# Performance work log

Hardware: AMD Instinct MI355X
Metric: run time of the kernel (lower is better)

Reference implementation:

```python
import jax, jax.numpy as jnp
import numpy as np

UNITS, N, S = 256, 64, 4
BATCH, T = 64, 1024


def setup_inputs() -> dict:
    key = jax.random.key(0)
    k0, k1, k2, k3 = jax.random.split(key, 4)
    return {
        "inputs": jax.random.uniform(k0, (BATCH, T, S), dtype=jnp.float32),
        "transition_kernel": jax.random.normal(k1, (UNITS, N, N), dtype=jnp.float32),
        "emission_kernel": jax.random.normal(k2, (UNITS, N, S), dtype=jnp.float32),
        "init_kernel": jax.random.normal(k3, (UNITS, N), dtype=jnp.float32),
    }


def reference(inputs, transition_kernel, emission_kernel, init_kernel):
    # Softmaxed HMM parameters (computed once; the TF cell recomputes per step).
    A = jax.nn.softmax(transition_kernel, axis=-1)  # [U, N, N] transitions
    B = jax.nn.softmax(emission_kernel, axis=-1)    # [U, N, S] emissions
    I = jax.nn.softmax(init_kernel, axis=-1)        # [U, N]    initial dist

    batch = inputs.shape[0]
    U, Nn = init_kernel.shape

    alpha0 = jnp.zeros((batch, U, Nn), dtype=inputs.dtype)
    ll0 = jnp.zeros((batch, U), dtype=inputs.dtype)
    is_init0 = jnp.ones((batch,), dtype=inputs.dtype)  # HMM starts in init at t=0

    def step(carry, x_t):
        alpha, ll, is_init = carry
        # R[b,u,j] = is_init[b]*I[u,j] + sum_i A[u,i,j]*alpha[b,u,i]  (A^T matvec)
        R = is_init[:, None, None] * I[None] + jnp.einsum("uij,bui->buj", A, alpha)
        # E[b,u,i] = sum_c B[u,i,c] * x_t[b,c]
        E = jnp.einsum("unc,bc->bun", B, x_t)
        fwd = E * R                              # [B, U, N]
        Ssum = jnp.sum(fwd, axis=-1)             # [B, U]
        ll = ll + jnp.log(Ssum)
        alpha = fwd / Ssum[..., None]            # normalized forward variable
        return (alpha, ll, jnp.zeros_like(is_init)), ll

    xs = jnp.swapaxes(inputs, 0, 1)  # [T, B, S]
    (_, _, _), lls = jax.lax.scan(step, (alpha0, ll0, is_init0), xs)
    # whole-sequence output: cumulative log-likelihood per step, [B, T, U]
    return jnp.swapaxes(lls, 0, 1)
```

## Files before the change

### kernel.cpp

```cpp
#include <hip/hip_runtime.h>


#define U_ 256
#define N_ 64
#define S_ 4
#define B_ 64
#define T_ 1024
#define ROWP 72

typedef __attribute__((ext_vector_type(8))) __bf16 bf16x8;
typedef __attribute__((ext_vector_type(4))) float floatx4;

__device__ __forceinline__ int sig(int jt, int m) {
    return 32 * (jt >> 1) + 4 * (jt & 1) + 8 * (m >> 2) + (m & 3);
}

__launch_bounds__(256, 1)
__global__ void hmm_fwd_kernel(const float* __restrict__ xg,
                               const float* __restrict__ trans,
                               const float* __restrict__ emis,
                               const float* __restrict__ initk,
                               float* __restrict__ out)
{
    __shared__ __bf16 AT[N_ * ROWP];
    __shared__ float BemS[N_][S_];
    __shared__ float IS[N_];

    const int bid = blockIdx.x;
    const int u = ((bid & 7) << 5) | (bid >> 3);
    const int tid = threadIdx.x;
    const int lane = tid & 63;
    const int w = tid >> 6;
    const int q = lane >> 4;
    const int l = lane & 15;

    if (tid < 64) {
        const float* rowp = trans + (u * N_ + tid) * N_;
        float v[N_];
        #pragma unroll
        for (int k = 0; k < 16; ++k) {
            floatx4 t4 = *(const floatx4*)(rowp + 4 * k);
            v[4*k] = t4.x; v[4*k+1] = t4.y; v[4*k+2] = t4.z; v[4*k+3] = t4.w;
        }
        float m = v[0];
        #pragma unroll
        for (int j = 1; j < N_; ++j) m = fmaxf(m, v[j]);
        float s = 0.f;
        #pragma unroll
        for (int j = 0; j < N_; ++j) { v[j] = __expf(v[j] - m); s += v[j]; }
        float inv = 1.0f / s;
        #pragma unroll
        for (int j = 0; j < N_; ++j) AT[j * ROWP + tid] = (__bf16)(v[j] * inv);
    } else if (tid < 128) {
        int n = tid - 64;
        floatx4 e4 = *(const floatx4*)(emis + (u * N_ + n) * S_);
        float m = fmaxf(fmaxf(e4.x, e4.y), fmaxf(e4.z, e4.w));
        float a = __expf(e4.x - m), b2 = __expf(e4.y - m);
        float c = __expf(e4.z - m), d = __expf(e4.w - m);
        float inv = 1.0f / (a + b2 + c + d);
        BemS[n][0] = a*inv; BemS[n][1] = b2*inv; BemS[n][2] = c*inv; BemS[n][3] = d*inv;
    } else if (tid < 192) {
        int j = tid - 128;
        float v = initk[u * N_ + j];
        float m = v;
        #pragma unroll
        for (int s = 1; s < 64; s <<= 1) m = fmaxf(m, __shfl_xor(m, s, 64));
        float e = __expf(v - m);
        float ssum = e;
        #pragma unroll
        for (int s = 1; s < 64; s <<= 1) ssum += __shfl_xor(ssum, s, 64);
        IS[j] = e / ssum;
    }
    __syncthreads();

    bf16x8 afrag[4][2];
    #pragma unroll
    for (int jt = 0; jt < 4; ++jt)
        #pragma unroll
        for (int kt = 0; kt < 2; ++kt)
            afrag[jt][kt] = *(const bf16x8*)&AT[sig(jt, l) * ROWP + 32*kt + 8*q];

    bf16x8 afragE[4];
    #pragma unroll
    for (int jt = 0; jt < 4; ++jt) {
        #pragma unroll
        for (int p = 0; p < 8; ++p) afragE[jt][p] = (__bf16)0.f;
        if (q == 0) {
            #pragma unroll
            for (int c = 0; c < 4; ++c)
                afragE[jt][c] = (__bf16)BemS[sig(jt, l)][c];
        }
    }

    floatx4 Rv[4];
    #pragma unroll
    for (int jt = 0; jt < 4; ++jt)
        #pragma unroll
        for (int r = 0; r < 4; ++r) Rv[jt][r] = IS[sig(jt, 4*q + r)];

    __asm__ volatile("" ::: "memory");

    const int b = 16*w + l;
    const float* xin = xg + b * (T_ * S_);
    float* outp = out + (size_t)b * T_ * U_ + u;

    const floatx4 z = {0.f, 0.f, 0.f, 0.f};
    floatx4 Ev[4], gv[4];
    float ll = 0.f, sp1 = 0.f, sp2 = 0.f, rsA = 1.0f;

    floatx4 x0 = *(const floatx4*)xin;
    floatx4 xA = *(const floatx4*)(xin + S_);
    floatx4 xB = *(const floatx4*)(xin + 2 * S_);

    {
        bf16x8 be;
        #pragma unroll
        for (int p = 0; p < 8; ++p) be[p] = (__bf16)0.f;
        if (q == 0) {
            be[0] = (__bf16)x0.x; be[1] = (__bf16)x0.y;
            be[2] = (__bf16)x0.z; be[3] = (__bf16)x0.w;
        }
        #pragma unroll
        for (int jt = 0; jt < 4; ++jt)
            Ev[jt] = __builtin_amdgcn_mfma_f32_16x16x32_bf16(afragE[jt], be, z, 0, 0, 0);
    }

    #pragma unroll 2
    for (int t = 0; t < T_; ++t) {
        #pragma unroll
        for (int jt = 0; jt < 4; ++jt) gv[jt] = Ev[jt] * Rv[jt];

        bf16x8 bf0, bf1;
        #pragma unroll
        for (int p = 0; p < 4; ++p) {
            bf0[p]     = (__bf16)gv[0][p];
            bf0[4 + p] = (__bf16)gv[1][p];
            bf1[p]     = (__bf16)gv[2][p];
            bf1[4 + p] = (__bf16)gv[3][p];
        }

        #pragma unroll
        for (int jt = 0; jt < 4; ++jt) {
            floatx4 acc = __builtin_amdgcn_mfma_f32_16x16x32_bf16(afrag[jt][0], bf0, z, 0, 0, 0);
            Rv[jt] = __builtin_amdgcn_mfma_f32_16x16x32_bf16(afrag[jt][1], bf1, acc, 0, 0, 0);
        }

        floatx4 s4 = (gv[0] + gv[1]) + (gv[2] + gv[3]);
        float p0 = (s4.x + s4.y) + (s4.z + s4.w);
        float a16 = __shfl_xor(p0, 16, 64);
        float a32 = __shfl_xor(p0, 32, 64);
        float a48 = __shfl_xor(p0, 48, 64);
        float ss = (p0 + a16) + (a32 + a48);
        float sg = __logf(ss);
        float rs = __builtin_amdgcn_rcpf(ss);

        ll += sg - sp1 + sp2;
        if (q == 0) outp[t * U_] = ll;
        sp2 = sp1; sp1 = sg;

        bf16x8 be;
        #pragma unroll
        for (int p = 0; p < 8; ++p) be[p] = (__bf16)0.f;
        if (q == 0) {
            floatx4 xs = xA * rsA;
            be[0] = (__bf16)xs.x; be[1] = (__bf16)xs.y;
            be[2] = (__bf16)xs.z; be[3] = (__bf16)xs.w;
        }
        #pragma unroll
        for (int jt = 0; jt < 4; ++jt)
            Ev[jt] = __builtin_amdgcn_mfma_f32_16x16x32_bf16(afragE[jt], be, z, 0, 0, 0);
        rsA = rs;

        xA = xB;
        int tp = (t + 3 < T_) ? t + 3 : T_ - 1;
        xB = *(const floatx4*)(xin + tp * S_);
    }
}

extern "C" void kernel_launch(void* const* d_in, const int* in_sizes, int n_in,
                              void* d_out, int out_size, void* d_ws, size_t ws_size,
                              hipStream_t stream) {
    const float* xg    = (const float*)d_in[0];
    const float* trans = (const float*)d_in[1];
    const float* emis  = (const float*)d_in[2];
    const float* initk = (const float*)d_in[3];
    float* out = (float*)d_out;
    hipLaunchKernelGGL(hmm_fwd_kernel, dim3(U_), dim3(256), 0, stream,
                       xg, trans, emis, initk, out);
}
```

Measured before the change: 362.2 us.

## Batch log-likelihood stores across quad lanes and block-prefetch inputs per 8 steps

Instead of q==0 lanes issuing one scattered store every timestep, each of the four lane quads keeps 8 consecutive ll values in a register history and writes them in a burst every 32 steps. This spreads the store work across all lanes and takes the per-step conditional store off the serial recurrence. Input x values are now prefetched four at a time in double-buffered groups, and the emission operand is built without the q==0 branch. The non-zero be entries in q!=0 lanes are multiplied by zero afragE entries, so results stay the same. Costs are extra registers for the history and prefetch buffers, and stores are deferred until the end of each 32-step group.

```diff
diff --git a/kernel.cpp b/kernel.cpp
--- a/kernel.cpp
+++ b/kernel.cpp
@@ -102,31 +102,35 @@
 
     const int b = 16*w + l;
     const float* xin = xg + b * (T_ * S_);
-    float* outp = out + (size_t)b * T_ * U_ + u;
+    float* llout = out + (size_t)b * T_ * U_ + u;
 
     const floatx4 z = {0.f, 0.f, 0.f, 0.f};
-    floatx4 Ev[4], gv[4];
+    floatx4 Ev[4];
     float ll = 0.f, sp1 = 0.f, sp2 = 0.f, rsA = 1.0f;
 
+    bf16x8 be;
+    #pragma unroll
+    for (int p = 0; p < 8; ++p) be[p] = (__bf16)0.f;
+
     floatx4 x0 = *(const floatx4*)xin;
-    floatx4 xA = *(const floatx4*)(xin + S_);
-    floatx4 xB = *(const floatx4*)(xin + 2 * S_);
+    floatx4 xvA[4], xvB[4];
+    #pragma unroll
+    for (int i = 0; i < 4; ++i)
+        xvA[i] = *(const floatx4*)(xin + (1 + i) * S_);
 
     {
-        bf16x8 be;
-        #pragma unroll
-        for (int p = 0; p < 8; ++p) be[p] = (__bf16)0.f;
-        if (q == 0) {
-            be[0] = (__bf16)x0.x; be[1] = (__bf16)x0.y;
-            be[2] = (__bf16)x0.z; be[3] = (__bf16)x0.w;
-        }
+        be[0] = (__bf16)x0.x; be[1] = (__bf16)x0.y;
+        be[2] = (__bf16)x0.z; be[3] = (__bf16)x0.w;
         #pragma unroll
         for (int jt = 0; jt < 4; ++jt)
             Ev[jt] = __builtin_amdgcn_mfma_f32_16x16x32_bf16(afragE[jt], be, z, 0, 0, 0);
     }
 
-    #pragma unroll 2
-    for (int t = 0; t < T_; ++t) {
+    float hist[8];
+    bool own = false;
+
+    auto step = [&](const floatx4& xsrc, int slot) {
+        floatx4 gv[4];
         #pragma unroll
         for (int jt = 0; jt < 4; ++jt) gv[jt] = Ev[jt] * Rv[jt];
 
@@ -155,25 +159,42 @@
         float rs = __builtin_amdgcn_rcpf(ss);
 
         ll += sg - sp1 + sp2;
-        if (q == 0) outp[t * U_] = ll;
         sp2 = sp1; sp1 = sg;
-
-        bf16x8 be;
-        #pragma unroll
-        for (int p = 0; p < 8; ++p) be[p] = (__bf16)0.f;
-        if (q == 0) {
-            floatx4 xs = xA * rsA;
-            be[0] = (__bf16)xs.x; be[1] = (__bf16)xs.y;
-            be[2] = (__bf16)xs.z; be[3] = (__bf16)xs.w;
-        }
+        hist[slot] = own ? ll : hist[slot];
+
+        floatx4 xs = xsrc * rsA;
+        be[0] = (__bf16)xs.x; be[1] = (__bf16)xs.y;
+        be[2] = (__bf16)xs.z; be[3] = (__bf16)xs.w;
         #pragma unroll
         for (int jt = 0; jt < 4; ++jt)
             Ev[jt] = __builtin_amdgcn_mfma_f32_16x16x32_bf16(afragE[jt], be, z, 0, 0, 0);
         rsA = rs;
-
-        xA = xB;
-        int tp = (t + 3 < T_) ? t + 3 : T_ - 1;
-        xB = *(const floatx4*)(xin + tp * S_);
+    };
+
+    for (int tb = 0; tb < T_; tb += 8) {
+        own = (q == ((tb >> 3) & 3));
+
+        #pragma unroll
+        for (int i = 0; i < 4; ++i) {
+            int ti = tb + 5 + i; ti = (ti < T_) ? ti : T_ - 1;
+            xvB[i] = *(const floatx4*)(xin + ti * S_);
+        }
+
+        step(xvA[0], 0); step(xvA[1], 1); step(xvA[2], 2); step(xvA[3], 3);
+
+        #pragma unroll
+        for (int i = 0; i < 4; ++i) {
+            int ti = tb + 9 + i; ti = (ti < T_) ? ti : T_ - 1;
+            xvA[i] = *(const floatx4*)(xin + ti * S_);
+        }
+
+        step(xvB[0], 4); step(xvB[1], 5); step(xvB[2], 6); step(xvB[3], 7);
+
+        if ((tb & 24) == 24) {
+            float* fp = llout + (size_t)((tb - 24) + 8 * q) * U_;
+            #pragma unroll
+            for (int k = 0; k < 8; ++k) fp[(size_t)k * U_] = hist[k];
+        }
     }
 }
 
```

Measured after the change: 371.3 us. +2.5%, slower.
